# Kernel optimization log

Measured on AMD Instinct MI355X. Metric: run time of the kernel, lower is better.

Reference implementation:

```python
import math
import jax, jax.numpy as jnp
import numpy as np

MODEL_DIM = 2048
NUM_EXPERTS = 64
NUM_TOKENS = 8192
CAPACITY_FACTOR = 1.0


def setup_inputs() -> dict:
    key = jax.random.key(0)
    kx, kw = jax.random.split(key)
    x = jax.random.normal(kx, (NUM_TOKENS, MODEL_DIM), dtype=jnp.float32)
    # Linear(model_dim, num_experts, bias=False): weight [E, D], y = x @ W.T
    wg = jax.random.normal(kw, (NUM_EXPERTS, MODEL_DIM), dtype=jnp.float32) * (1.0 / math.sqrt(MODEL_DIM))
    return {"x": x, "wg": wg}


def reference(x, wg):
    # ---- gate projection: logits [S, E] ----
    logits = jnp.einsum('sd,ed->se', x, wg)
    gates = jax.nn.softmax(logits, axis=1)
    S, E = gates.shape
    # training mode -> capacity = capacity_factor * ceil(S / E)  (static)
    capacity = int(CAPACITY_FACTOR * math.ceil(S / E))

    # ---- top-1 expert selection ----
    indices1_s = jnp.argmax(gates, axis=1)                      # [S]
    mask1 = jax.nn.one_hot(indices1_s, E, dtype=jnp.int32)      # [S, E]

    # gate value of the chosen expert per token
    gates1_s = jnp.sum(gates * mask1.astype(gates.dtype), axis=1)  # [S]

    # position of each token within its expert's queue (cumsum over tokens)
    locations1 = jnp.cumsum(mask1, axis=0) - 1                  # [S, E]

    # ---- load-balancing auxiliary loss ----
    me = jnp.mean(gates, axis=0)                                # [E]
    ce = jnp.mean(mask1.astype(gates.dtype), axis=0)            # [E]
    l_aux = jnp.mean(me * ce) * (E * E)

    # ---- capacity enforcement: drop tokens beyond expert capacity ----
    mask1 = mask1 * (locations1 < capacity).astype(mask1.dtype) # [S, E]
    locations1_s = jnp.sum(locations1 * mask1, axis=1)          # [S]

    # ---- combine / dispatch tensors ----
    gates1 = gates1_s[:, None] * mask1.astype(gates.dtype)      # [S, E]
    locations1_sc = jax.nn.one_hot(locations1_s, capacity, dtype=gates.dtype)  # [S, C]
    # torch.bmm(gates1[:, :, None], locations1_sc[:, None, :]) == outer product per token
    combine1_sec = jnp.einsum('se,sc->sec', gates1, locations1_sc)  # [S, E, C]
    dispatch_mask = combine1_sec > 0                            # bool [S, E, C]

    return l_aux, combine1_sec, dispatch_mask
```

## Files before the change

kernel.cpp:

```cpp
#include <hip/hip_runtime.h>
#include <math.h>

#define DIM     2048
#define NEXP    64
#define CAP     128
#define NTOK    8192
#define NTILE   256
#define KC      256
#define NCH     (DIM/KC)
#define XWSTR   260
#define PSTR    68
#define RF      67108864

typedef float vfloat4 __attribute__((ext_vector_type(4)));

__global__ __launch_bounds__(256) void fill_out(float* __restrict__ out)
{
    vfloat4* o4 = reinterpret_cast<vfloat4*>(out);
    const vfloat4 z4 = {0.f, 0.f, 0.f, 0.f};
    size_t base = (size_t)blockIdx.x * 8192 + threadIdx.x;
    #pragma unroll
    for (int q = 0; q < 32; ++q)
        o4[base + ((size_t)q << 8)] = z4;
    if (blockIdx.x == 0 && threadIdx.x == 0)
        out[134217728ull] = 0.0f;
}

__global__ __launch_bounds__(512, 2) void gate_kernel(
    const float* __restrict__ x, const float* __restrict__ wg,
    int* __restrict__ expert_idx, float* __restrict__ gate_top,
    int* __restrict__ rank,
    float* __restrict__ me_partial, int* __restrict__ counts)
{
    __shared__ __align__(16) float smem[(32 + NEXP) * XWSTR];
    __shared__ float me_w[8 * NEXP];
    __shared__ int   cnt_w[8 * NEXP];
    __shared__ int   exp_s[32];

    float* xs = smem;
    float* ws = smem + 32 * XWSTR;

    const int tid  = threadIdx.x;
    const int gb   = blockIdx.x;
    const int tok0 = gb * 32;
    const int sl   = tid >> 5;
    const int i    = tid & 31;
    const int tg   = i & 3;
    const int eg   = i >> 2;
    const int kb   = sl * 16;

    float acc[8][8] = {};

    for (int ch = 0; ch < NCH; ++ch) {
        const int k0 = ch * KC;
        #pragma unroll
        for (int q = 0; q < 4; ++q) {
            int id = tid + (q << 9);
            int r = id >> 6, c = id & 63;
            float4 v = *(const float4*)(x + (size_t)(tok0 + r) * DIM + k0 + 4 * c);
            *(float4*)(&xs[r * XWSTR + 4 * c]) = v;
        }
        #pragma unroll
        for (int q = 0; q < 8; ++q) {
            int id = tid + (q << 9);
            int r = id >> 6, c = id & 63;
            float4 v = *(const float4*)(wg + (size_t)r * DIM + k0 + 4 * c);
            *(float4*)(&ws[r * XWSTR + 4 * c]) = v;
        }
        __syncthreads();

        #pragma unroll
        for (int q2 = 0; q2 < 4; ++q2) {
            const int kk = kb + 4 * q2;
            float4 xt[8], we[8];
            #pragma unroll
            for (int j = 0; j < 8; ++j)
                xt[j] = *(const float4*)(&xs[(tg + 4 * j) * XWSTR + kk]);
            #pragma unroll
            for (int m = 0; m < 8; ++m)
                we[m] = *(const float4*)(&ws[(eg + 8 * m) * XWSTR + kk]);
            #pragma unroll
            for (int j = 0; j < 8; ++j)
                #pragma unroll
                for (int m = 0; m < 8; ++m) {
                    acc[j][m] = fmaf(xt[j].x, we[m].x, acc[j][m]);
                    acc[j][m] = fmaf(xt[j].y, we[m].y, acc[j][m]);
                    acc[j][m] = fmaf(xt[j].z, we[m].z, acc[j][m]);
                    acc[j][m] = fmaf(xt[j].w, we[m].w, acc[j][m]);
                }
        }
        __syncthreads();
    }

    float* part = smem;
    float* lgt  = smem + 8 * 32 * PSTR;
    if (sl >= 8) {
        #pragma unroll
        for (int j = 0; j < 8; ++j)
            #pragma unroll
            for (int m = 0; m < 8; ++m)
                part[((sl - 8) * 32 + tg + 4 * j) * PSTR + eg + 8 * m] = acc[j][m];
    }
    __syncthreads();
    if (sl < 8) {
        #pragma unroll
        for (int j = 0; j < 8; ++j)
            #pragma unroll
            for (int m = 0; m < 8; ++m) {
                int idx = (sl * 32 + tg + 4 * j) * PSTR + eg + 8 * m;
                part[idx] += acc[j][m];
            }
    }
    __syncthreads();

    {
        int t  = tid >> 4;
        int e0 = (tid & 15) << 2;
        float4 a = {0, 0, 0, 0};
        #pragma unroll
        for (int s2 = 0; s2 < 8; ++s2) {
            float4 p = *(const float4*)(&part[(s2 * 32 + t) * PSTR + e0]);
            a.x += p.x; a.y += p.y; a.z += p.z; a.w += p.w;
        }
        *(float4*)(&lgt[t * PSTR + e0]) = a;
    }
    __syncthreads();

    const int lane = tid & 63;
    const int wv   = tid >> 6;
    float me_acc  = 0.0f;
    int   cnt_acc = 0;
    #pragma unroll
    for (int r4 = 0; r4 < 4; ++r4) {
        int row = wv * 4 + r4;
        float v = lgt[row * PSTR + lane];
        float m = v; int mi = lane;
        #pragma unroll
        for (int off = 32; off > 0; off >>= 1) {
            float om  = __shfl_xor(m, off);
            int   omi = __shfl_xor(mi, off);
            if (om > m || (om == m && omi < mi)) { m = om; mi = omi; }
        }
        float ex = __expf(v - m);
        float sm = ex;
        #pragma unroll
        for (int off = 32; off > 0; off >>= 1) sm += __shfl_xor(sm, off);
        me_acc += ex / sm;
        if (lane == mi) {
            expert_idx[tok0 + row] = mi;
            gate_top[tok0 + row]   = 1.0f / sm;
            exp_s[row] = mi;
            ++cnt_acc;
        }
    }
    me_w[wv * NEXP + lane]  = me_acc;
    cnt_w[wv * NEXP + lane] = cnt_acc;
    __syncthreads();

    if (tid < 32) {
        int e = exp_s[tid];
        int rk = 0;
        for (int u = 0; u < tid; ++u) rk += (exp_s[u] == e) ? 1 : 0;
        rank[tok0 + tid] = rk;
    }
    if (tid < NEXP) {
        float ms = 0.f; int cs = 0;
        #pragma unroll
        for (int w = 0; w < 8; ++w) { ms += me_w[w * NEXP + tid]; cs += cnt_w[w * NEXP + tid]; }
        me_partial[gb * NEXP + tid] = ms;
        counts[gb * NEXP + tid]     = cs;
    }
}

__global__ __launch_bounds__(1024) void prefix_laux(
    const float* __restrict__ me_partial, const int* __restrict__ counts,
    const int* __restrict__ expert_idx, const int* __restrict__ rank,
    const float* __restrict__ gate_top, float* __restrict__ out)
{
    __shared__ int   bo_l[NTILE * NEXP];
    __shared__ int   cnt_l[16 * NEXP];
    __shared__ float me_l[16 * NEXP];
    __shared__ int   cnt_tot[NEXP];
    __shared__ float me_tot[NEXP];

    const int tid = threadIdx.x;
    const int e   = tid & 63;
    const int g   = tid >> 6;

    int cs = 0; float ms = 0.f;
    #pragma unroll
    for (int i = 0; i < 16; ++i) {
        int t = g * 16 + i;
        cs += counts[t * NEXP + e];
        ms += me_partial[t * NEXP + e];
    }
    cnt_l[g * NEXP + e] = cs;
    me_l[g * NEXP + e]  = ms;
    __syncthreads();

    if (g == 0) {
        int run = 0; float mt = 0.f;
        #pragma unroll
        for (int i = 0; i < 16; ++i) {
            int c = cnt_l[i * NEXP + e];
            cnt_l[i * NEXP + e] = run;
            run += c;
            mt  += me_l[i * NEXP + e];
        }
        cnt_tot[e] = run;
        me_tot[e]  = mt;
    }
    __syncthreads();

    int run = cnt_l[g * NEXP + e];
    #pragma unroll
    for (int i = 0; i < 16; ++i) {
        int t = g * 16 + i;
        bo_l[t * NEXP + e] = run;
        run += counts[t * NEXP + e];
    }
    __syncthreads();

    if (tid < NEXP) {
        float v = (me_tot[e] / (float)NTOK) * ((float)cnt_tot[e] / (float)NTOK);
        #pragma unroll
        for (int off = 32; off > 0; off >>= 1) v += __shfl_xor(v, off);
        if (e == 0) out[0] = v * (float)NEXP;
    }

    #pragma unroll
    for (int ii = 0; ii < 8; ++ii) {
        int s  = tid + (ii << 10);
        int ex = expert_idx[s];
        int loc = bo_l[(s >> 5) * NEXP + ex] + rank[s];
        if (loc < CAP) {
            size_t off = 1 + (size_t)s * (NEXP * CAP) + (size_t)ex * CAP + loc;
            out[off]              = gate_top[s];
            out[off + (size_t)RF] = 1.0f;
        }
    }
}

extern "C" void kernel_launch(void* const* d_in, const int* in_sizes, int n_in,
                              void* d_out, int out_size, void* d_ws, size_t ws_size,
                              hipStream_t stream)
{
    const float* x  = (const float*)d_in[0];
    const float* wg = (const float*)d_in[1];
    float* out = (float*)d_out;

    char* ws = (char*)d_ws;
    int*   expert_idx = (int*)  (ws);
    float* gate_top   = (float*)(ws + 32768);
    int*   rank       = (int*)  (ws + 65536);
    float* me_partial = (float*)(ws + 98304);
    int*   counts     = (int*)  (ws + 163840);

    fill_out<<<4096, 256, 0, stream>>>(out);
    gate_kernel<<<NTILE, 512, 0, stream>>>(x, wg, expert_idx, gate_top, rank,
                                           me_partial, counts);
    prefix_laux<<<1, 1024, 0, stream>>>(me_partial, counts, expert_idx, rank,
                                        gate_top, out);
}
```

Measured before the change: 628.2 us.

## Fuse zero-fill into gate kernel grid and halve K-chunk size

The separate zero-fill kernel is folded into the gate GEMM launch as extra blocks, so the large output memset can run alongside the gate projection instead of before it. The K-chunk drops from 256 to 128, which shrinks shared memory per block and should allow more resident blocks, at the cost of twice as many sync rounds. The partial-sum reduction becomes a four-stage accumulation into a smaller buffer to fit the reduced LDS. Fill blocks now write 16384 float4s each with 512 threads over 2048 blocks, still covering the whole output.

```diff
diff --git a/kernel.cpp b/kernel.cpp
--- a/kernel.cpp
+++ b/kernel.cpp
@@ -6,28 +6,19 @@
 #define CAP     128
 #define NTOK    8192
 #define NTILE   256
-#define KC      256
+#define KC      128
 #define NCH     (DIM/KC)
-#define XWSTR   260
+#define XWSTR   132
 #define PSTR    68
 #define RF      67108864
+#define NFILL   2048
+#define GRID    (NTILE + NFILL)
 
 typedef float vfloat4 __attribute__((ext_vector_type(4)));
 
-__global__ __launch_bounds__(256) void fill_out(float* __restrict__ out)
-{
-    vfloat4* o4 = reinterpret_cast<vfloat4*>(out);
-    const vfloat4 z4 = {0.f, 0.f, 0.f, 0.f};
-    size_t base = (size_t)blockIdx.x * 8192 + threadIdx.x;
-    #pragma unroll
-    for (int q = 0; q < 32; ++q)
-        o4[base + ((size_t)q << 8)] = z4;
-    if (blockIdx.x == 0 && threadIdx.x == 0)
-        out[134217728ull] = 0.0f;
-}
-
-__global__ __launch_bounds__(512, 2) void gate_kernel(
+__global__ __launch_bounds__(512, 2) void fused_gate(
     const float* __restrict__ x, const float* __restrict__ wg,
+    float* __restrict__ out,
     int* __restrict__ expert_idx, float* __restrict__ gate_top,
     int* __restrict__ rank,
     float* __restrict__ me_partial, int* __restrict__ counts)
@@ -37,40 +28,55 @@
     __shared__ int   cnt_w[8 * NEXP];
     __shared__ int   exp_s[32];
 
+    const int tid = threadIdx.x;
+    const int b   = blockIdx.x;
+
+    if (b >= NTILE) {
+        const int zb = b - NTILE;
+        vfloat4* o4 = reinterpret_cast<vfloat4*>(out);
+        const vfloat4 z4 = {0.f, 0.f, 0.f, 0.f};
+        size_t base = (size_t)zb * 16384 + tid;
+        #pragma unroll
+        for (int q = 0; q < 32; ++q)
+            o4[base + ((size_t)q << 9)] = z4;
+        if (zb == 0 && tid == 0)
+            out[134217728ull] = 0.0f;
+        return;
+    }
+
     float* xs = smem;
     float* ws = smem + 32 * XWSTR;
 
-    const int tid  = threadIdx.x;
-    const int gb   = blockIdx.x;
+    const int gb   = b;
     const int tok0 = gb * 32;
     const int sl   = tid >> 5;
     const int i    = tid & 31;
     const int tg   = i & 3;
     const int eg   = i >> 2;
-    const int kb   = sl * 16;
+    const int kb   = sl * 8;
 
     float acc[8][8] = {};
 
     for (int ch = 0; ch < NCH; ++ch) {
         const int k0 = ch * KC;
         #pragma unroll
+        for (int q = 0; q < 2; ++q) {
+            int id = tid + (q << 9);
+            int r = id >> 5, c = id & 31;
+            float4 v = *(const float4*)(x + (size_t)(tok0 + r) * DIM + k0 + 4 * c);
+            *(float4*)(&xs[r * XWSTR + 4 * c]) = v;
+        }
+        #pragma unroll
         for (int q = 0; q < 4; ++q) {
             int id = tid + (q << 9);
-            int r = id >> 6, c = id & 63;
-            float4 v = *(const float4*)(x + (size_t)(tok0 + r) * DIM + k0 + 4 * c);
-            *(float4*)(&xs[r * XWSTR + 4 * c]) = v;
-        }
-        #pragma unroll
-        for (int q = 0; q < 8; ++q) {
-            int id = tid + (q << 9);
-            int r = id >> 6, c = id & 63;
+            int r = id >> 5, c = id & 31;
             float4 v = *(const float4*)(wg + (size_t)r * DIM + k0 + 4 * c);
             *(float4*)(&ws[r * XWSTR + 4 * c]) = v;
         }
         __syncthreads();
 
         #pragma unroll
-        for (int q2 = 0; q2 < 4; ++q2) {
+        for (int q2 = 0; q2 < 2; ++q2) {
             const int kk = kb + 4 * q2;
             float4 xt[8], we[8];
             #pragma unroll
@@ -93,23 +99,37 @@
     }
 
     float* part = smem;
-    float* lgt  = smem + 8 * 32 * PSTR;
-    if (sl >= 8) {
-        #pragma unroll
-        for (int j = 0; j < 8; ++j)
-            #pragma unroll
-            for (int m = 0; m < 8; ++m)
-                part[((sl - 8) * 32 + tg + 4 * j) * PSTR + eg + 8 * m] = acc[j][m];
-    }
-    __syncthreads();
-    if (sl < 8) {
-        #pragma unroll
-        for (int j = 0; j < 8; ++j)
-            #pragma unroll
-            for (int m = 0; m < 8; ++m) {
-                int idx = (sl * 32 + tg + 4 * j) * PSTR + eg + 8 * m;
-                part[idx] += acc[j][m];
-            }
+    float* lgt  = smem + 4 * 32 * PSTR;
+    if (sl >= 12) {
+        #pragma unroll
+        for (int j = 0; j < 8; ++j)
+            #pragma unroll
+            for (int m = 0; m < 8; ++m)
+                part[((sl - 12) * 32 + tg + 4 * j) * PSTR + eg + 8 * m] = acc[j][m];
+    }
+    __syncthreads();
+    if (sl >= 8 && sl < 12) {
+        #pragma unroll
+        for (int j = 0; j < 8; ++j)
+            #pragma unroll
+            for (int m = 0; m < 8; ++m)
+                part[((sl - 8) * 32 + tg + 4 * j) * PSTR + eg + 8 * m] += acc[j][m];
+    }
+    __syncthreads();
+    if (sl >= 4 && sl < 8) {
+        #pragma unroll
+        for (int j = 0; j < 8; ++j)
+            #pragma unroll
+            for (int m = 0; m < 8; ++m)
+                part[((sl - 4) * 32 + tg + 4 * j) * PSTR + eg + 8 * m] += acc[j][m];
+    }
+    __syncthreads();
+    if (sl < 4) {
+        #pragma unroll
+        for (int j = 0; j < 8; ++j)
+            #pragma unroll
+            for (int m = 0; m < 8; ++m)
+                part[(sl * 32 + tg + 4 * j) * PSTR + eg + 8 * m] += acc[j][m];
     }
     __syncthreads();
 
@@ -118,7 +138,7 @@
         int e0 = (tid & 15) << 2;
         float4 a = {0, 0, 0, 0};
         #pragma unroll
-        for (int s2 = 0; s2 < 8; ++s2) {
+        for (int s2 = 0; s2 < 4; ++s2) {
             float4 p = *(const float4*)(&part[(s2 * 32 + t) * PSTR + e0]);
             a.x += p.x; a.y += p.y; a.z += p.z; a.w += p.w;
         }
@@ -256,9 +276,8 @@
     float* me_partial = (float*)(ws + 98304);
     int*   counts     = (int*)  (ws + 163840);
 
-    fill_out<<<4096, 256, 0, stream>>>(out);
-    gate_kernel<<<NTILE, 512, 0, stream>>>(x, wg, expert_idx, gate_top, rank,
-                                           me_partial, counts);
+    fused_gate<<<GRID, 512, 0, stream>>>(x, wg, out, expert_idx, gate_top,
+                                         rank, me_partial, counts);
     prefix_laux<<<1, 1024, 0, stream>>>(me_partial, counts, expert_idx, rank,
                                         gate_top, out);
 }
```

After: 629.3 us. No clear change (+0.2%).
